# Kernel optimization log

Measured on AMD Instinct MI355X. Metric: run time of the kernel, lower is better.

Reference implementation:

```python
import jax, jax.numpy as jnp
from jax import lax
import numpy as np

D = 1024   # hidden_size
N = 8      # num_experts
K = 2      # num_chosen_experts
KS = 1     # num_shared_experts
H = 2 * D  # hidden_ratio * D
B, S = 2, 1024


def setup_inputs() -> dict:
    key = jax.random.key(0)
    k1, k2, k3, k4 = jax.random.split(key, 4)
    scale = 1.0 / np.sqrt(D).astype(np.float32)
    x = jax.random.normal(k1, (B, S, D), dtype=jnp.float32)
    Wg = jax.random.normal(k2, (D, N), dtype=jnp.float32) * scale
    Wl1 = jax.random.normal(k3, (N, D, 2 * H), dtype=jnp.float32) * scale
    Wl2 = jax.random.normal(k4, (N, H, D), dtype=jnp.float32) * scale
    return {"x_BSD": x, "Wg_DN": Wg, "Wl1_ND2H": Wl1, "Wl2_NHD": Wl2}


def _moe(x_BSD, Wg_DN, Wl1_ND2H, Wl2_NHD):
    b, s, d = x_BSD.shape
    x_MD = x_BSD.reshape(b * s, d)            # [M, D]
    Nr = N - KS                               # number of routed experts

    # --- gating (softmax path) ---
    s_raw_MN = x_MD @ Wg_DN                   # [M, N]
    routed = jax.nn.softmax(s_raw_MN[:, :Nr].astype(jnp.float32), axis=-1)
    shared = jax.nn.softmax(s_raw_MN[:, Nr:].astype(jnp.float32), axis=-1)

    # biases for routed experts are zero at init -> topk on raw softmax scores
    _, idx_MK = lax.top_k(routed, K - KS)     # [M, K-KS]
    mask = jnp.sum(jax.nn.one_hot(idx_MK, Nr, dtype=jnp.float32), axis=1)  # [M, Nr]
    sel = routed * mask
    routed_n = sel / jnp.sum(sel, axis=-1, keepdims=True)   # renormalize selected gates
    shared_n = shared / jnp.sum(shared, axis=-1, keepdims=True)
    gates_MN = jnp.concatenate([routed_n, shared_n], axis=-1).astype(x_MD.dtype)  # [M, N]

    # --- experts: gather-free dense combine; gates are exactly 0 for unselected experts ---
    def step(y_MD, inp):
        w1_D2H, w2_HD, g_M = inp
        z = x_MD @ w1_D2H                     # [M, 2H]
        a, bgate = jnp.split(z, 2, axis=-1)
        h = jax.nn.silu(bgate) * a            # SwiGLU
        return y_MD + g_M[:, None] * (h @ w2_HD), None

    y0 = jnp.zeros_like(x_MD)
    y_MD, _ = lax.scan(step, y0, (Wl1_ND2H, Wl2_NHD, gates_MN.T))
    return y_MD.reshape(b, s, d)


def reference(x_BSD, Wg_DN, Wl1_ND2H, Wl2_NHD):
    return _moe(x_BSD, Wg_DN, Wl1_ND2H, Wl2_NHD)
```

## Files before the change

### kernel.cpp

```cpp
#include <hip/hip_runtime.h>
#include <stdint.h>


typedef __bf16 bf16x8 __attribute__((ext_vector_type(8)));
typedef float f32x4 __attribute__((ext_vector_type(4)));

typedef __attribute__((address_space(1))) const void gvoid_t;
typedef __attribute__((address_space(3))) void lvoid_t;

__device__ __forceinline__ void gload16(void* lds, const void* g) {
  __builtin_amdgcn_global_load_lds((gvoid_t*)g, (lvoid_t*)lds, 16, 0, 0);
}

__device__ __forceinline__ uint16_t f2bf(float f) {
  union { float f; uint32_t u; } v; v.f = f;
  uint32_t u = v.u + 0x7fffu + ((v.u >> 16) & 1u);
  return (uint16_t)(u >> 16);
}

#define S_VMCNT12() asm volatile("s_waitcnt vmcnt(12)" ::: "memory")
#define S_VMCNT16() asm volatile("s_waitcnt vmcnt(16)" ::: "memory")
#define S_VMCNT0()  asm volatile("s_waitcnt vmcnt(0)" ::: "memory")
#define S_LGKM0()   asm volatile("s_waitcnt lgkmcnt(0)" ::: "memory")
#define S_BAR()     __builtin_amdgcn_s_barrier()

#define CVT_PK(dst, lo, hi) \
  asm("v_cvt_pk_bf16_f32 %0, %1, %2" : "=v"(dst) : "v"(lo), "v"(hi))

__global__ __launch_bounds__(256) void gate_kernel(const float* __restrict__ x,
                                                   const float* __restrict__ Wg,
                                                   uint16_t* __restrict__ xbf,
                                                   int* __restrict__ idx) {
  int wid = threadIdx.x >> 6, lane = threadIdx.x & 63;
  int m = blockIdx.x * 4 + wid;
  const float* xr = x + (size_t)m * 1024;
  uint16_t* xbr = xbf + (size_t)m * 1024;
  float acc[8] = {0.f, 0.f, 0.f, 0.f, 0.f, 0.f, 0.f, 0.f};
  for (int it = 0; it < 4; ++it) {
    int dbase = it * 256 + lane * 4;
    float4 xv = *reinterpret_cast<const float4*>(xr + dbase);
    ushort4 o;
    o.x = f2bf(xv.x); o.y = f2bf(xv.y); o.z = f2bf(xv.z); o.w = f2bf(xv.w);
    *reinterpret_cast<ushort4*>(xbr + dbase) = o;
    const float* xp = reinterpret_cast<const float*>(&xv);
    for (int dd = 0; dd < 4; ++dd) {
      float xs = xp[dd];
      float4 w0 = *reinterpret_cast<const float4*>(Wg + (size_t)(dbase + dd) * 8);
      float4 w1 = *reinterpret_cast<const float4*>(Wg + (size_t)(dbase + dd) * 8 + 4);
      acc[0] += xs * w0.x; acc[1] += xs * w0.y; acc[2] += xs * w0.z; acc[3] += xs * w0.w;
      acc[4] += xs * w1.x; acc[5] += xs * w1.y; acc[6] += xs * w1.z; acc[7] += xs * w1.w;
    }
  }
  for (int j = 0; j < 7; ++j)
    for (int off = 32; off; off >>= 1)
      acc[j] += __shfl_xor(acc[j], off);
  if (lane == 0) {
    int best = 0; float bv = acc[0];
    for (int j = 1; j < 7; ++j) if (acc[j] > bv) { bv = acc[j]; best = j; }
    idx[m] = best;
  }
}

__global__ __launch_bounds__(256) void compact_kernel(const int* __restrict__ idx,
                                                      int* __restrict__ soff,
                                                      int* __restrict__ scnt,
                                                      int* __restrict__ rowmap,
                                                      int* __restrict__ tokrow) {
  __shared__ int hist[256][7];
  __shared__ int cnts[7];
  __shared__ int off[7];
  int t = threadIdx.x;
  int e8[8];
  int lh[7] = {0, 0, 0, 0, 0, 0, 0};
#pragma unroll
  for (int i = 0; i < 8; ++i) { int e = idx[t * 8 + i]; e8[i] = e; lh[e]++; }
#pragma unroll
  for (int e = 0; e < 7; ++e) hist[t][e] = lh[e];
  __syncthreads();
  if (t < 7) {
    int run = 0;
    for (int i = 0; i < 256; ++i) { int v = hist[i][t]; hist[i][t] = run; run += v; }
    cnts[t] = run;
  }
  __syncthreads();
  if (t == 0) {
    int run = 0;
    for (int e = 0; e < 7; ++e) { off[e] = run; soff[e] = run; scnt[e] = cnts[e]; run += cnts[e]; }
    soff[7] = 0; scnt[7] = 2048;
  }
  __syncthreads();
  int pos[7];
#pragma unroll
  for (int e = 0; e < 7; ++e) pos[e] = off[e] + hist[t][e];
#pragma unroll
  for (int i = 0; i < 8; ++i) {
    int m = t * 8 + i, e = e8[i];
    int r = pos[e]++;
    rowmap[r] = m;
    tokrow[m] = r;
  }
}

__global__ __launch_bounds__(256, 2) void ffn1_kernel(
    const uint16_t* __restrict__ xbf,
    const float* __restrict__ W1,
    const int* __restrict__ soff, const int* __restrict__ scnt,
    const int* __restrict__ rowmap,
    uint16_t* __restrict__ h)
{
  int by = blockIdx.y;
  int seg, rt;
  if (by < 42) { seg = by / 6; rt = by % 6; } else { seg = 7; rt = by - 42; }
  int cnt = scnt[seg];
  if (rt * 128 >= cnt) return;
  int base = (seg == 7) ? 2048 : soff[seg];
  int rbase = (seg == 7) ? 0 : soff[seg];
  int bx = blockIdx.x;

  __shared__ uint16_t lds[2][16384];

  int t = threadIdx.x, lane = t & 63, w = t >> 6;
  int trow = w * 8 + ((t >> 3) & 7);
  int slot = (t & 7) ^ (trow & 7);

  const uint16_t* aptr[4];
#pragma unroll
  for (int i = 0; i < 4; ++i) {
    int rl = i * 32 + trow;
    int rr = rt * 128 + rl; if (rr >= cnt) rr = cnt - 1;
    int tok = (seg == 7) ? rr : rowmap[rbase + rr];
    aptr[i] = xbf + (size_t)tok * 1024 + slot * 8;
  }
  auto stageA = [&](int buf, int kt) {
    uint16_t* L = lds[buf];
#pragma unroll
    for (int i = 0; i < 4; ++i) gload16(&L[(i * 32 + trow) * 64 + (t & 7) * 8], aptr[i] + kt * 64);
  };

  const float* w1f = W1 + (size_t)seg * (1024u * 4096u);
  int kg = t >> 5;
  int n4 = (t & 31) * 4;
  int gcol = (n4 >> 5) * 1024 + bx * 32 + (n4 & 31);
  const float* bsrc = w1f + (size_t)(kg * 8) * 4096 + gcol;
  int bwoff[4];
#pragma unroll
  for (int j = 0; j < 4; ++j) {
    int cl = n4 + j;
    int sw = cl ^ ((cl >> 2) & 7);
    bwoff[j] = 8192 + kg * 1024 + sw * 8;
  }
  f32x4 P0[8], P1[8];
  auto issueB = [&](f32x4 (&P)[8], int kt) {
    const float* p = bsrc + (size_t)kt * 64 * 4096;
#pragma unroll
    for (int i = 0; i < 8; ++i) P[i] = *reinterpret_cast<const f32x4*>(p + (size_t)i * 4096);
  };
  auto writeB = [&](f32x4 (&P)[8], int buf) {
    uint16_t* L = lds[buf];
#pragma unroll
    for (int j = 0; j < 4; ++j) {
      uint32_t q0, q1, q2, q3;
      CVT_PK(q0, P[0][j], P[1][j]);
      CVT_PK(q1, P[2][j], P[3][j]);
      CVT_PK(q2, P[4][j], P[5][j]);
      CVT_PK(q3, P[6][j], P[7][j]);
      uint4 v; v.x = q0; v.y = q1; v.z = q2; v.w = q3;
      *reinterpret_cast<uint4*>(&L[bwoff[j]]) = v;
    }
  };

  int wr = (w >> 1) & 1, wc = w & 1;
  int l15 = lane & 15, lk = lane >> 4;
  int boffA[2], boffB[2];
#pragma unroll
  for (int n = 0; n < 2; ++n) {
    int cl = wc * 32 + n * 16 + l15;
    boffA[n] = 8192 + (cl ^ ((cl >> 2) & 7)) * 8;
    int cb = cl + 64;
    boffB[n] = 8192 + (cb ^ ((cb >> 2) & 7)) * 8;
  }

  f32x4 acca[4][2] = {};
  f32x4 accb[4][2] = {};

  auto compute = [&](int buf) {
    const uint16_t* L = lds[buf];
#pragma unroll
    for (int g = 0; g < 2; ++g) {
      __builtin_amdgcn_s_setprio(1);
      bf16x8 af[4];
#pragma unroll
      for (int m = 0; m < 4; ++m) {
        int row = wr * 64 + m * 16 + l15;
        int p = (g * 4 + lk) ^ (row & 7);
        af[m] = *reinterpret_cast<const bf16x8*>(&L[row * 64 + p * 8]);
      }
#pragma unroll
      for (int n = 0; n < 2; ++n) {
        int ks = (g * 4 + lk) * 1024;
        bf16x8 ba = *reinterpret_cast<const bf16x8*>(&L[boffA[n] + ks]);
        bf16x8 bb = *reinterpret_cast<const bf16x8*>(&L[boffB[n] + ks]);
#pragma unroll
        for (int m = 0; m < 4; ++m) {
          acca[m][n] = __builtin_amdgcn_mfma_f32_16x16x32_bf16(af[m], ba, acca[m][n], 0, 0, 0);
          accb[m][n] = __builtin_amdgcn_mfma_f32_16x16x32_bf16(af[m], bb, accb[m][n], 0, 0, 0);
        }
      }
      __builtin_amdgcn_s_setprio(0);
    }
  };

  const int NT = 16;
  issueB(P0, 0); stageA(0, 0);
  issueB(P1, 1); stageA(1, 1);
  S_VMCNT16();
  writeB(P0, 0);
  issueB(P0, 2);
  S_LGKM0();

#pragma unroll 1
  for (int kt = 0; kt < NT; kt += 2) {
    if (kt < NT - 2) S_VMCNT12(); else S_VMCNT0();
    S_BAR();
    compute(0);
    if (kt < NT - 1) writeB(P1, 1);
    S_LGKM0(); S_BAR();
    if (kt < NT - 3) issueB(P1, kt + 3);
    if (kt < NT - 2) stageA(0, kt + 2);
    int ko = kt + 1;
    if (ko < NT - 2) S_VMCNT12(); else S_VMCNT0();
    S_BAR();
    compute(1);
    if (ko < NT - 1) writeB(P0, 0);
    S_LGKM0(); S_BAR();
    if (ko < NT - 3) issueB(P0, ko + 3);
    if (ko < NT - 2) stageA(1, ko + 2);
  }

#pragma unroll
  for (int m = 0; m < 4; ++m)
#pragma unroll
    for (int n = 0; n < 2; ++n) {
      int cl = wc * 32 + n * 16 + l15;
      int col = (cl >> 5) * 1024 + bx * 32 + (cl & 31);
#pragma unroll
      for (int j = 0; j < 4; ++j) {
        int row = rt * 128 + wr * 64 + m * 16 + lk * 4 + j;
        if (row < cnt) {
          float a = acca[m][n][j], b = accb[m][n][j];
          float sv = b / (1.0f + __expf(-b));
          h[(size_t)(base + row) * 2048 + col] = f2bf(sv * a);
        }
      }
    }
}

__global__ __launch_bounds__(256, 2) void ffn2_kernel(
    const uint16_t* __restrict__ h,
    const float* __restrict__ W2,
    const int* __restrict__ soff, const int* __restrict__ scnt,
    float* __restrict__ y, float* __restrict__ yr)
{
  int by = blockIdx.y;
  int seg, rt;
  if (by < 42) { seg = by / 6; rt = by % 6; } else { seg = 7; rt = by - 42; }
  int cnt = scnt[seg];
  if (rt * 128 >= cnt) return;
  int base = (seg == 7) ? 2048 : soff[seg];
  int obase = (seg == 7) ? 0 : soff[seg];
  int n0 = blockIdx.x * 128;

  __shared__ uint16_t lds[2][16384];

  int t = threadIdx.x, lane = t & 63, w = t >> 6;
  int trow = w * 8 + ((t >> 3) & 7);
  int slot = (t & 7) ^ (trow & 7);

  const uint16_t* aptr[4];
#pragma unroll
  for (int i = 0; i < 4; ++i) {
    int rl = i * 32 + trow;
    int rr = rt * 128 + rl; if (rr >= cnt) rr = cnt - 1;
    aptr[i] = h + (size_t)(base + rr) * 2048 + slot * 8;
  }
  auto stageA = [&](int buf, int kt) {
    uint16_t* L = lds[buf];
#pragma unroll
    for (int i = 0; i < 4; ++i) gload16(&L[(i * 32 + trow) * 64 + (t & 7) * 8], aptr[i] + kt * 64);
  };

  const float* w2f = W2 + (size_t)seg * (2048u * 1024u);
  int kg = t >> 5;
  int n4 = (t & 31) * 4;
  const float* bsrc = w2f + (size_t)(kg * 8) * 1024 + n0 + n4;
  int bwoff[4];
#pragma unroll
  for (int j = 0; j < 4; ++j) {
    int cl = n4 + j;
    int sw = cl ^ ((cl >> 2) & 7);
    bwoff[j] = 8192 + kg * 1024 + sw * 8;
  }
  f32x4 P0[8], P1[8];
  auto issueB = [&](f32x4 (&P)[8], int kt) {
    const float* p = bsrc + (size_t)kt * 64 * 1024;
#pragma unroll
    for (int i = 0; i < 8; ++i) P[i] = *reinterpret_cast<const f32x4*>(p + (size_t)i * 1024);
  };
  auto writeB = [&](f32x4 (&P)[8], int buf) {
    uint16_t* L = lds[buf];
#pragma unroll
    for (int j = 0; j < 4; ++j) {
      uint32_t q0, q1, q2, q3;
      CVT_PK(q0, P[0][j], P[1][j]);
      CVT_PK(q1, P[2][j], P[3][j]);
      CVT_PK(q2, P[4][j], P[5][j]);
      CVT_PK(q3, P[6][j], P[7][j]);
      uint4 v; v.x = q0; v.y = q1; v.z = q2; v.w = q3;
      *reinterpret_cast<uint4*>(&L[bwoff[j]]) = v;
    }
  };

  int wr = (w >> 1) & 1, wc = w & 1;
  int l15 = lane & 15, lk = lane >> 4;
  int boff[4];
#pragma unroll
  for (int n = 0; n < 4; ++n) {
    int cl = wc * 64 + n * 16 + l15;
    boff[n] = 8192 + (cl ^ ((cl >> 2) & 7)) * 8;
  }

  f32x4 acc[4][4] = {};

  auto compute = [&](int buf) {
    const uint16_t* L = lds[buf];
#pragma unroll
    for (int g = 0; g < 2; ++g) {
      __builtin_amdgcn_s_setprio(1);
      bf16x8 af[4];
#pragma unroll
      for (int m = 0; m < 4; ++m) {
        int row = wr * 64 + m * 16 + l15;
        int p = (g * 4 + lk) ^ (row & 7);
        af[m] = *reinterpret_cast<const bf16x8*>(&L[row * 64 + p * 8]);
      }
#pragma unroll
      for (int n = 0; n < 4; ++n) {
        bf16x8 bfr = *reinterpret_cast<const bf16x8*>(&L[boff[n] + (g * 4 + lk) * 1024]);
#pragma unroll
        for (int m = 0; m < 4; ++m)
          acc[m][n] = __builtin_amdgcn_mfma_f32_16x16x32_bf16(af[m], bfr, acc[m][n], 0, 0, 0);
      }
      __builtin_amdgcn_s_setprio(0);
    }
  };

  const int NT = 32;
  issueB(P0, 0); stageA(0, 0);
  issueB(P1, 1); stageA(1, 1);
  S_VMCNT16();
  writeB(P0, 0);
  issueB(P0, 2);
  S_LGKM0();

#pragma unroll 1
  for (int kt = 0; kt < NT; kt += 2) {
    if (kt < NT - 2) S_VMCNT12(); else S_VMCNT0();
    S_BAR();
    compute(0);
    if (kt < NT - 1) writeB(P1, 1);
    S_LGKM0(); S_BAR();
    if (kt < NT - 3) issueB(P1, kt + 3);
    if (kt < NT - 2) stageA(0, kt + 2);
    int ko = kt + 1;
    if (ko < NT - 2) S_VMCNT12(); else S_VMCNT0();
    S_BAR();
    compute(1);
    if (ko < NT - 1) writeB(P0, 0);
    S_LGKM0(); S_BAR();
    if (ko < NT - 3) issueB(P0, ko + 3);
    if (ko < NT - 2) stageA(1, ko + 2);
  }

#pragma unroll
  for (int m = 0; m < 4; ++m)
#pragma unroll
    for (int n = 0; n < 4; ++n) {
      int col = n0 + wc * 64 + n * 16 + l15;
#pragma unroll
      for (int j = 0; j < 4; ++j) {
        int row = rt * 128 + wr * 64 + m * 16 + lk * 4 + j;
        if (row < cnt) {
          if (seg == 7) y[(size_t)row * 1024 + col] = acc[m][n][j];
          else          yr[(size_t)(obase + row) * 1024 + col] = acc[m][n][j];
        }
      }
    }
}

__global__ __launch_bounds__(256) void combine_kernel(const float* __restrict__ yr,
                                                      const int* __restrict__ tokrow,
                                                      float* __restrict__ y) {
  int m = blockIdx.x;
  int d = threadIdx.x * 4;
  int r = tokrow[m];
  float4 a = *reinterpret_cast<const float4*>(yr + (size_t)r * 1024 + d);
  float4 o = *reinterpret_cast<const float4*>(y + (size_t)m * 1024 + d);
  o.x += a.x; o.y += a.y; o.z += a.z; o.w += a.w;
  *reinterpret_cast<float4*>(y + (size_t)m * 1024 + d) = o;
}

extern "C" void kernel_launch(void* const* d_in, const int* in_sizes, int n_in,
                              void* d_out, int out_size, void* d_ws, size_t ws_size,
                              hipStream_t stream)
{
  const float* x   = (const float*)d_in[0];
  const float* Wg  = (const float*)d_in[1];
  const float* Wl1 = (const float*)d_in[2];
  const float* Wl2 = (const float*)d_in[3];
  float* y = (float*)d_out;
  char* ws = (char*)d_ws;

  uint16_t* xbf = (uint16_t*)(ws);
  uint16_t* h   = (uint16_t*)(ws + (4ull  << 20));
  float*    yr  = (float*)   (ws + (20ull << 20));
  int* idx    = (int*)(ws + (28ull << 20));
  int* tokrow = idx + 2048;
  int* soff   = tokrow + 2048;
  int* scnt   = soff + 8;
  int* rowmap = scnt + 8;

  gate_kernel<<<512, 256, 0, stream>>>(x, Wg, xbf, idx);
  compact_kernel<<<1, 256, 0, stream>>>(idx, soff, scnt, rowmap, tokrow);
  ffn1_kernel<<<dim3(32, 58), 256, 0, stream>>>(xbf, Wl1, soff, scnt, rowmap, h);
  ffn2_kernel<<<dim3(8, 58), 256, 0, stream>>>(h, Wl2, soff, scnt, y, yr);
  combine_kernel<<<2048, 256, 0, stream>>>(yr, tokrow, y);
}
```

Baseline: 131.1 us.

## Pre-convert W1 to bf16 in a separate kernel before the FFN1 GEMM

Adds a conversion kernel that turns the full fp32 W1 into a bf16 copy in the workspace on every call. ffn1 then loads bf16 weights instead of fp32, using a new thread-to-tile mapping with byte permutes into the same swizzled LDS layout, and waits on fewer outstanding loads. The aim is to halve the W1 bytes ffn1 fetches and drop its in-loop fp32-to-bf16 conversion, since each expert's weights are re-read by several row tiles. In exchange it adds a full pass that reads 128MB and writes 64MB of bf16 per call, plus a larger workspace.

```diff
diff --git a/kernel.cpp b/kernel.cpp
--- a/kernel.cpp
+++ b/kernel.cpp
@@ -18,6 +18,7 @@
   return (uint16_t)(u >> 16);
 }
 
+#define S_VMCNT8()  asm volatile("s_waitcnt vmcnt(8)" ::: "memory")
 #define S_VMCNT12() asm volatile("s_waitcnt vmcnt(12)" ::: "memory")
 #define S_VMCNT16() asm volatile("s_waitcnt vmcnt(16)" ::: "memory")
 #define S_VMCNT0()  asm volatile("s_waitcnt vmcnt(0)" ::: "memory")
@@ -26,6 +27,25 @@
 
 #define CVT_PK(dst, lo, hi) \
   asm("v_cvt_pk_bf16_f32 %0, %1, %2" : "=v"(dst) : "v"(lo), "v"(hi))
+
+__global__ __launch_bounds__(256) void cvt1_kernel(const float* __restrict__ W1,
+                                                   uint16_t* __restrict__ w1c) {
+  size_t i0 = ((size_t)blockIdx.x * 256 + threadIdx.x) * 8;
+  const f32x4* src = reinterpret_cast<const f32x4*>(W1);
+  uint4* dst = reinterpret_cast<uint4*>(w1c);
+#pragma unroll
+  for (int j = 0; j < 4; ++j) {
+    f32x4 a = src[i0 + 2 * j];
+    f32x4 b = src[i0 + 2 * j + 1];
+    uint32_t q0, q1, q2, q3;
+    CVT_PK(q0, a[0], a[1]);
+    CVT_PK(q1, a[2], a[3]);
+    CVT_PK(q2, b[0], b[1]);
+    CVT_PK(q3, b[2], b[3]);
+    uint4 v; v.x = q0; v.y = q1; v.z = q2; v.w = q3;
+    dst[i0 / 2 + j] = v;
+  }
+}
 
 __global__ __launch_bounds__(256) void gate_kernel(const float* __restrict__ x,
                                                    const float* __restrict__ Wg,
@@ -103,7 +123,7 @@
 
 __global__ __launch_bounds__(256, 2) void ffn1_kernel(
     const uint16_t* __restrict__ xbf,
-    const float* __restrict__ W1,
+    const uint16_t* __restrict__ w1c,
     const int* __restrict__ soff, const int* __restrict__ scnt,
     const int* __restrict__ rowmap,
     uint16_t* __restrict__ h)
@@ -115,7 +135,7 @@
   if (rt * 128 >= cnt) return;
   int base = (seg == 7) ? 2048 : soff[seg];
   int rbase = (seg == 7) ? 0 : soff[seg];
-  int bx = blockIdx.x;
+  int n0 = blockIdx.x * 64;
 
   __shared__ uint16_t lds[2][16384];
 
@@ -137,11 +157,165 @@
     for (int i = 0; i < 4; ++i) gload16(&L[(i * 32 + trow) * 64 + (t & 7) * 8], aptr[i] + kt * 64);
   };
 
-  const float* w1f = W1 + (size_t)seg * (1024u * 4096u);
+  const uint16_t* w1e = w1c + (size_t)seg * (1024u * 4096u);
+  int kg = (t >> 4) & 7;
+  int khalf = t >> 7;
+  int colc = (t & 15) * 8;
+  int gcol = (colc < 64) ? (n0 + colc) : (2048 + n0 + colc - 64);
+  const uint16_t* bsrc = w1e + (size_t)(kg * 8 + khalf * 4) * 4096 + gcol;
+  int bwoff[8];
+#pragma unroll
+  for (int j = 0; j < 8; ++j) {
+    int cl = colc + j;
+    int sw = cl ^ ((cl >> 2) & 7);
+    bwoff[j] = 8192 + kg * 1024 + sw * 8 + khalf * 4;
+  }
+  uint4 P0[4], P1[4];
+  auto issueB = [&](uint4 (&P)[4], int kt) {
+    const uint16_t* p = bsrc + (size_t)kt * 64 * 4096;
+#pragma unroll
+    for (int i = 0; i < 4; ++i) P[i] = *reinterpret_cast<const uint4*>(p + (size_t)i * 4096);
+  };
+  auto writeB = [&](uint4 (&P)[4], int buf) {
+    uint16_t* L = lds[buf];
+    const uint32_t* p0 = reinterpret_cast<const uint32_t*>(&P[0]);
+    const uint32_t* p1 = reinterpret_cast<const uint32_t*>(&P[1]);
+    const uint32_t* p2 = reinterpret_cast<const uint32_t*>(&P[2]);
+    const uint32_t* p3 = reinterpret_cast<const uint32_t*>(&P[3]);
+#pragma unroll
+    for (int j = 0; j < 8; ++j) {
+      int wd = j >> 1;
+      uint32_t selv = (j & 1) ? 0x07060302u : 0x05040100u;
+      uint32_t lo = __builtin_amdgcn_perm(p1[wd], p0[wd], selv);
+      uint32_t hi = __builtin_amdgcn_perm(p3[wd], p2[wd], selv);
+      uint2 v; v.x = lo; v.y = hi;
+      *reinterpret_cast<uint2*>(&L[bwoff[j]]) = v;
+    }
+  };
+
+  int wr = (w >> 1) & 1, wc = w & 1;
+  int l15 = lane & 15, lk = lane >> 4;
+  int boffA[2], boffB[2];
+#pragma unroll
+  for (int n = 0; n < 2; ++n) {
+    int cl = wc * 32 + n * 16 + l15;
+    boffA[n] = 8192 + (cl ^ ((cl >> 2) & 7)) * 8;
+    int cb = cl + 64;
+    boffB[n] = 8192 + (cb ^ ((cb >> 2) & 7)) * 8;
+  }
+
+  f32x4 acca[4][2] = {};
+  f32x4 accb[4][2] = {};
+
+  auto compute = [&](int buf) {
+    const uint16_t* L = lds[buf];
+#pragma unroll
+    for (int g = 0; g < 2; ++g) {
+      __builtin_amdgcn_s_setprio(1);
+      bf16x8 af[4];
+#pragma unroll
+      for (int m = 0; m < 4; ++m) {
+        int row = wr * 64 + m * 16 + l15;
+        int p = (g * 4 + lk) ^ (row & 7);
+        af[m] = *reinterpret_cast<const bf16x8*>(&L[row * 64 + p * 8]);
+      }
+#pragma unroll
+      for (int n = 0; n < 2; ++n) {
+        int ks = (g * 4 + lk) * 1024;
+        bf16x8 ba = *reinterpret_cast<const bf16x8*>(&L[boffA[n] + ks]);
+        bf16x8 bb = *reinterpret_cast<const bf16x8*>(&L[boffB[n] + ks]);
+#pragma unroll
+        for (int m = 0; m < 4; ++m) {
+          acca[m][n] = __builtin_amdgcn_mfma_f32_16x16x32_bf16(af[m], ba, acca[m][n], 0, 0, 0);
+          accb[m][n] = __builtin_amdgcn_mfma_f32_16x16x32_bf16(af[m], bb, accb[m][n], 0, 0, 0);
+        }
+      }
+      __builtin_amdgcn_s_setprio(0);
+    }
+  };
+
+  const int NT = 16;
+  issueB(P0, 0); stageA(0, 0);
+  issueB(P1, 1); stageA(1, 1);
+  S_VMCNT12();
+  writeB(P0, 0);
+  issueB(P0, 2);
+  S_LGKM0();
+
+#pragma unroll 1
+  for (int kt = 0; kt < NT; kt += 2) {
+    if (kt < NT - 2) S_VMCNT8(); else S_VMCNT0();
+    S_BAR();
+    compute(0);
+    if (kt < NT - 1) writeB(P1, 1);
+    S_LGKM0(); S_BAR();
+    if (kt < NT - 3) issueB(P1, kt + 3);
+    if (kt < NT - 2) stageA(0, kt + 2);
+    int ko = kt + 1;
+    if (ko < NT - 2) S_VMCNT8(); else S_VMCNT0();
+    S_BAR();
+    compute(1);
+    if (ko < NT - 1) writeB(P0, 0);
+    S_LGKM0(); S_BAR();
+    if (ko < NT - 3) issueB(P0, ko + 3);
+    if (ko < NT - 2) stageA(1, ko + 2);
+  }
+
+#pragma unroll
+  for (int m = 0; m < 4; ++m)
+#pragma unroll
+    for (int n = 0; n < 2; ++n) {
+      int col = n0 + wc * 32 + n * 16 + l15;
+#pragma unroll
+      for (int j = 0; j < 4; ++j) {
+        int row = rt * 128 + wr * 64 + m * 16 + lk * 4 + j;
+        if (row < cnt) {
+          float a = acca[m][n][j], b = accb[m][n][j];
+          float sv = b / (1.0f + __expf(-b));
+          h[(size_t)(base + row) * 2048 + col] = f2bf(sv * a);
+        }
+      }
+    }
+}
+
+__global__ __launch_bounds__(256, 2) void ffn2_kernel(
+    const uint16_t* __restrict__ h,
+    const float* __restrict__ W2,
+    const int* __restrict__ soff, const int* __restrict__ scnt,
+    float* __restrict__ y, float* __restrict__ yr)
+{
+  int by = blockIdx.y;
+  int seg, rt;
+  if (by < 42) { seg = by / 6; rt = by % 6; } else { seg = 7; rt = by - 42; }
+  int cnt = scnt[seg];
+  if (rt * 128 >= cnt) return;
+  int base = (seg == 7) ? 2048 : soff[seg];
+  int obase = (seg == 7) ? 0 : soff[seg];
+  int n0 = blockIdx.x * 128;
+
+  __shared__ uint16_t lds[2][16384];
+
+  int t = threadIdx.x, lane = t & 63, w = t >> 6;
+  int trow = w * 8 + ((t >> 3) & 7);
+  int slot = (t & 7) ^ (trow & 7);
+
+  const uint16_t* aptr[4];
+#pragma unroll
+  for (int i = 0; i < 4; ++i) {
+    int rl = i * 32 + trow;
+    int rr = rt * 128 + rl; if (rr >= cnt) rr = cnt - 1;
+    aptr[i] = h + (size_t)(base + rr) * 2048 + slot * 8;
+  }
+  auto stageA = [&](int buf, int kt) {
+    uint16_t* L = lds[buf];
+#pragma unroll
+    for (int i = 0; i < 4; ++i) gload16(&L[(i * 32 + trow) * 64 + (t & 7) * 8], aptr[i] + kt * 64);
+  };
+
+  const float* w2f = W2 + (size_t)seg * (2048u * 1024u);
   int kg = t >> 5;
   int n4 = (t & 31) * 4;
-  int gcol = (n4 >> 5) * 1024 + bx * 32 + (n4 & 31);
-  const float* bsrc = w1f + (size_t)(kg * 8) * 4096 + gcol;
+  const float* bsrc = w2f + (size_t)(kg * 8) * 1024 + n0 + n4;
   int bwoff[4];
 #pragma unroll
   for (int j = 0; j < 4; ++j) {
@@ -151,9 +325,9 @@
   }
   f32x4 P0[8], P1[8];
   auto issueB = [&](f32x4 (&P)[8], int kt) {
-    const float* p = bsrc + (size_t)kt * 64 * 4096;
-#pragma unroll
-    for (int i = 0; i < 8; ++i) P[i] = *reinterpret_cast<const f32x4*>(p + (size_t)i * 4096);
+    const float* p = bsrc + (size_t)kt * 64 * 1024;
+#pragma unroll
+    for (int i = 0; i < 8; ++i) P[i] = *reinterpret_cast<const f32x4*>(p + (size_t)i * 1024);
   };
   auto writeB = [&](f32x4 (&P)[8], int buf) {
     uint16_t* L = lds[buf];
@@ -171,17 +345,14 @@
 
   int wr = (w >> 1) & 1, wc = w & 1;
   int l15 = lane & 15, lk = lane >> 4;
-  int boffA[2], boffB[2];
-#pragma unroll
-  for (int n = 0; n < 2; ++n) {
-    int cl = wc * 32 + n * 16 + l15;
-    boffA[n] = 8192 + (cl ^ ((cl >> 2) & 7)) * 8;
-    int cb = cl + 64;
-    boffB[n] = 8192 + (cb ^ ((cb >> 2) & 7)) * 8;
-  }
-
-  f32x4 acca[4][2] = {};
-  f32x4 accb[4][2] = {};
+  int boff[4];
+#pragma unroll
+  for (int n = 0; n < 4; ++n) {
+    int cl = wc * 64 + n * 16 + l15;
+    boff[n] = 8192 + (cl ^ ((cl >> 2) & 7)) * 8;
+  }
+
+  f32x4 acc[4][4] = {};
 
   auto compute = [&](int buf) {
     const uint16_t* L = lds[buf];
@@ -196,21 +367,17 @@
         af[m] = *reinterpret_cast<const bf16x8*>(&L[row * 64 + p * 8]);
       }
 #pragma unroll
-      for (int n = 0; n < 2; ++n) {
-        int ks = (g * 4 + lk) * 1024;
-        bf16x8 ba = *reinterpret_cast<const bf16x8*>(&L[boffA[n] + ks]);
-        bf16x8 bb = *reinterpret_cast<const bf16x8*>(&L[boffB[n] + ks]);
-#pragma unroll
-        for (int m = 0; m < 4; ++m) {
-          acca[m][n] = __builtin_amdgcn_mfma_f32_16x16x32_bf16(af[m], ba, acca[m][n], 0, 0, 0);
-          accb[m][n] = __builtin_amdgcn_mfma_f32_16x16x32_bf16(af[m], bb, accb[m][n], 0, 0, 0);
-        }
+      for (int n = 0; n < 4; ++n) {
+        bf16x8 bfr = *reinterpret_cast<const bf16x8*>(&L[boff[n] + (g * 4 + lk) * 1024]);
+#pragma unroll
+        for (int m = 0; m < 4; ++m)
+          acc[m][n] = __builtin_amdgcn_mfma_f32_16x16x32_bf16(af[m], bfr, acc[m][n], 0, 0, 0);
       }
       __builtin_amdgcn_s_setprio(0);
     }
   };
 
-  const int NT = 16;
+  const int NT = 32;
   issueB(P0, 0); stageA(0, 0);
   issueB(P1, 1); stageA(1, 1);
   S_VMCNT16();
@@ -240,150 +407,6 @@
 #pragma unroll
   for (int m = 0; m < 4; ++m)
 #pragma unroll
-    for (int n = 0; n < 2; ++n) {
-      int cl = wc * 32 + n * 16 + l15;
-      int col = (cl >> 5) * 1024 + bx * 32 + (cl & 31);
-#pragma unroll
-      for (int j = 0; j < 4; ++j) {
-        int row = rt * 128 + wr * 64 + m * 16 + lk * 4 + j;
-        if (row < cnt) {
-          float a = acca[m][n][j], b = accb[m][n][j];
-          float sv = b / (1.0f + __expf(-b));
-          h[(size_t)(base + row) * 2048 + col] = f2bf(sv * a);
-        }
-      }
-    }
-}
-
-__global__ __launch_bounds__(256, 2) void ffn2_kernel(
-    const uint16_t* __restrict__ h,
-    const float* __restrict__ W2,
-    const int* __restrict__ soff, const int* __restrict__ scnt,
-    float* __restrict__ y, float* __restrict__ yr)
-{
-  int by = blockIdx.y;
-  int seg, rt;
-  if (by < 42) { seg = by / 6; rt = by % 6; } else { seg = 7; rt = by - 42; }
-  int cnt = scnt[seg];
-  if (rt * 128 >= cnt) return;
-  int base = (seg == 7) ? 2048 : soff[seg];
-  int obase = (seg == 7) ? 0 : soff[seg];
-  int n0 = blockIdx.x * 128;
-
-  __shared__ uint16_t lds[2][16384];
-
-  int t = threadIdx.x, lane = t & 63, w = t >> 6;
-  int trow = w * 8 + ((t >> 3) & 7);
-  int slot = (t & 7) ^ (trow & 7);
-
-  const uint16_t* aptr[4];
-#pragma unroll
-  for (int i = 0; i < 4; ++i) {
-    int rl = i * 32 + trow;
-    int rr = rt * 128 + rl; if (rr >= cnt) rr = cnt - 1;
-    aptr[i] = h + (size_t)(base + rr) * 2048 + slot * 8;
-  }
-  auto stageA = [&](int buf, int kt) {
-    uint16_t* L = lds[buf];
-#pragma unroll
-    for (int i = 0; i < 4; ++i) gload16(&L[(i * 32 + trow) * 64 + (t & 7) * 8], aptr[i] + kt * 64);
-  };
-
-  const float* w2f = W2 + (size_t)seg * (2048u * 1024u);
-  int kg = t >> 5;
-  int n4 = (t & 31) * 4;
-  const float* bsrc = w2f + (size_t)(kg * 8) * 1024 + n0 + n4;
-  int bwoff[4];
-#pragma unroll
-  for (int j = 0; j < 4; ++j) {
-    int cl = n4 + j;
-    int sw = cl ^ ((cl >> 2) & 7);
-    bwoff[j] = 8192 + kg * 1024 + sw * 8;
-  }
-  f32x4 P0[8], P1[8];
-  auto issueB = [&](f32x4 (&P)[8], int kt) {
-    const float* p = bsrc + (size_t)kt * 64 * 1024;
-#pragma unroll
-    for (int i = 0; i < 8; ++i) P[i] = *reinterpret_cast<const f32x4*>(p + (size_t)i * 1024);
-  };
-  auto writeB = [&](f32x4 (&P)[8], int buf) {
-    uint16_t* L = lds[buf];
-#pragma unroll
-    for (int j = 0; j < 4; ++j) {
-      uint32_t q0, q1, q2, q3;
-      CVT_PK(q0, P[0][j], P[1][j]);
-      CVT_PK(q1, P[2][j], P[3][j]);
-      CVT_PK(q2, P[4][j], P[5][j]);
-      CVT_PK(q3, P[6][j], P[7][j]);
-      uint4 v; v.x = q0; v.y = q1; v.z = q2; v.w = q3;
-      *reinterpret_cast<uint4*>(&L[bwoff[j]]) = v;
-    }
-  };
-
-  int wr = (w >> 1) & 1, wc = w & 1;
-  int l15 = lane & 15, lk = lane >> 4;
-  int boff[4];
-#pragma unroll
-  for (int n = 0; n < 4; ++n) {
-    int cl = wc * 64 + n * 16 + l15;
-    boff[n] = 8192 + (cl ^ ((cl >> 2) & 7)) * 8;
-  }
-
-  f32x4 acc[4][4] = {};
-
-  auto compute = [&](int buf) {
-    const uint16_t* L = lds[buf];
-#pragma unroll
-    for (int g = 0; g < 2; ++g) {
-      __builtin_amdgcn_s_setprio(1);
-      bf16x8 af[4];
-#pragma unroll
-      for (int m = 0; m < 4; ++m) {
-        int row = wr * 64 + m * 16 + l15;
-        int p = (g * 4 + lk) ^ (row & 7);
-        af[m] = *reinterpret_cast<const bf16x8*>(&L[row * 64 + p * 8]);
-      }
-#pragma unroll
-      for (int n = 0; n < 4; ++n) {
-        bf16x8 bfr = *reinterpret_cast<const bf16x8*>(&L[boff[n] + (g * 4 + lk) * 1024]);
-#pragma unroll
-        for (int m = 0; m < 4; ++m)
-          acc[m][n] = __builtin_amdgcn_mfma_f32_16x16x32_bf16(af[m], bfr, acc[m][n], 0, 0, 0);
-      }
-      __builtin_amdgcn_s_setprio(0);
-    }
-  };
-
-  const int NT = 32;
-  issueB(P0, 0); stageA(0, 0);
-  issueB(P1, 1); stageA(1, 1);
-  S_VMCNT16();
-  writeB(P0, 0);
-  issueB(P0, 2);
-  S_LGKM0();
-
-#pragma unroll 1
-  for (int kt = 0; kt < NT; kt += 2) {
-    if (kt < NT - 2) S_VMCNT12(); else S_VMCNT0();
-    S_BAR();
-    compute(0);
-    if (kt < NT - 1) writeB(P1, 1);
-    S_LGKM0(); S_BAR();
-    if (kt < NT - 3) issueB(P1, kt + 3);
-    if (kt < NT - 2) stageA(0, kt + 2);
-    int ko = kt + 1;
-    if (ko < NT - 2) S_VMCNT12(); else S_VMCNT0();
-    S_BAR();
-    compute(1);
-    if (ko < NT - 1) writeB(P0, 0);
-    S_LGKM0(); S_BAR();
-    if (ko < NT - 3) issueB(P0, ko + 3);
-    if (ko < NT - 2) stageA(1, ko + 2);
-  }
-
-#pragma unroll
-  for (int m = 0; m < 4; ++m)
-#pragma unroll
     for (int n = 0; n < 4; ++n) {
       int col = n0 + wc * 64 + n * 16 + l15;
 #pragma unroll
@@ -423,7 +446,8 @@
   uint16_t* xbf = (uint16_t*)(ws);
   uint16_t* h   = (uint16_t*)(ws + (4ull  << 20));
   float*    yr  = (float*)   (ws + (20ull << 20));
-  int* idx    = (int*)(ws + (28ull << 20));
+  uint16_t* w1c = (uint16_t*)(ws + (28ull << 20));
+  int* idx    = (int*)(ws + (92ull << 20));
   int* tokrow = idx + 2048;
   int* soff   = tokrow + 2048;
   int* scnt   = soff + 8;
@@ -431,7 +455,8 @@
 
   gate_kernel<<<512, 256, 0, stream>>>(x, Wg, xbf, idx);
   compact_kernel<<<1, 256, 0, stream>>>(idx, soff, scnt, rowmap, tokrow);
-  ffn1_kernel<<<dim3(32, 58), 256, 0, stream>>>(xbf, Wl1, soff, scnt, rowmap, h);
+  cvt1_kernel<<<4096, 256, 0, stream>>>(Wl1, w1c);
+  ffn1_kernel<<<dim3(32, 58), 256, 0, stream>>>(xbf, w1c, soff, scnt, rowmap, h);
   ffn2_kernel<<<dim3(8, 58), 256, 0, stream>>>(h, Wl2, soff, scnt, y, yr);
   combine_kernel<<<2048, 256, 0, stream>>>(yr, tokrow, y);
 }
```

New measurement: 187.3 us. 1.43x slower.
